# Kernel optimization log

Measured on AMD Instinct MI355X. Metric: run time of the kernel, lower is better.

## Reference

```python
import jax, jax.numpy as jnp
import numpy as np


def _hardswish(x):
    return x * jnp.clip(x + 3.0, 0.0, 6.0) / 6.0


def _rel_coords_table(W):
    # [1, 2W-1, 2W-1, 2], log-spaced continuous relative coords (SwinV2)
    rc = jnp.arange(-(W - 1), W, dtype=jnp.float32)
    grid = jnp.stack(jnp.meshgrid(rc, rc, indexing='ij'), axis=-1)[None]
    grid = grid / float(W - 1) * 8.0
    return jnp.sign(grid) * jnp.log2(jnp.abs(grid) + 1.0) / np.float32(np.log2(8.0))


def _rel_pos_index(W):
    # [N, N] int indices into the (2W-1)^2 bias table
    coords = np.stack(np.meshgrid(np.arange(W), np.arange(W), indexing='ij')).reshape(2, -1)
    rel = (coords[:, :, None] - coords[:, None, :]).transpose(1, 2, 0)  # [N, N, 2]
    rel[:, :, 0] += W - 1
    rel[:, :, 1] += W - 1
    rel[:, :, 0] *= 2 * W - 1
    return jnp.asarray(rel.sum(-1))


def setup_inputs() -> dict:
    key = jax.random.key(0)
    ks = jax.random.split(key, 6)
    dim, num_heads, W = 512, 16, 8
    N = W * W
    B, nW = 2048, 64
    return {
        'x': jax.random.normal(ks[0], (B, N, dim), jnp.float32),
        'mask': jax.random.normal(ks[1], (nW, N, N), jnp.float32),
        'w_qkv': jax.random.normal(ks[2], (dim, 3 * dim), jnp.float32) * 0.02,
        'w_out': jax.random.normal(ks[3], (dim, dim), jnp.float32) * 0.02,
        'cpb_w1': jax.random.normal(ks[4], (2, 512), jnp.float32) * 0.02,
        'cpb_w2': jax.random.normal(ks[5], (512, num_heads), jnp.float32) * 0.02,
        'logits_scale': jnp.log(10.0 * jnp.ones((num_heads, 1, 1), jnp.float32)),
        'window_size': W,
        'num_heads': num_heads,
    }


def reference(x, mask, w_qkv, w_out, cpb_w1, cpb_w2, logits_scale, window_size, num_heads):
    B, N, C = x.shape
    hd = C // num_heads
    qkv = (x @ w_qkv).reshape(B, N, 3, num_heads, hd).transpose(2, 0, 3, 1, 4)
    q, k, v = qkv[0], qkv[1], qkv[2]  # [B, H, N, hd]

    # cosine attention (L2-normalized q, k) with clamped learned logit scale
    qn = q / jnp.clip(jnp.linalg.norm(q, axis=-1, keepdims=True), 1e-12)
    kn = k / jnp.clip(jnp.linalg.norm(k, axis=-1, keepdims=True), 1e-12)
    attn = jnp.einsum('bhnd,bhmd->bhnm', qn, kn)
    scale = jnp.exp(jnp.minimum(logits_scale, jnp.log(jnp.float32(100.0))))  # [H,1,1]
    attn = attn * scale[None]

    # continuous position bias via tiny MLP + index gather, sigmoid-scaled
    table = _rel_coords_table(window_size)                       # [1, 2W-1, 2W-1, 2]
    bias_table = (_hardswish(table @ cpb_w1) @ cpb_w2).reshape(-1, num_heads)
    idx = _rel_pos_index(window_size)                            # [N, N]
    bias = bias_table[idx.reshape(-1)].reshape(N, N, num_heads).transpose(2, 0, 1)
    attn = attn + 16.0 * jax.nn.sigmoid(bias)[None]

    if mask is not None:
        nW = mask.shape[0]
        attn = attn.reshape(B // nW, nW, num_heads, N, N) + mask[None, :, None]
        attn = attn.reshape(B, num_heads, N, N)

    # NOTE: original uses nn.Softmax(1) -> softmax over the HEAD axis; replicate faithfully
    attn = jax.nn.softmax(attn, axis=1)

    out = jnp.einsum('bhnm,bhmd->bhnd', attn, v).transpose(0, 2, 1, 3).reshape(B, N, C)
    return out @ w_out
```

## Files before the change

### kernel.cpp

```cpp
#include <hip/hip_runtime.h>
#include <hip/hip_bf16.h>

typedef unsigned short u16;
typedef unsigned int u32;
typedef __attribute__((ext_vector_type(8))) short bf16x8;
typedef __attribute__((ext_vector_type(4))) float f32x4;
typedef __attribute__((ext_vector_type(4))) float float4v;

__device__ __forceinline__ float bf2f(u16 v) {
  union { u32 u; float f; } x; x.u = ((u32)v) << 16; return x.f;
}
__device__ __forceinline__ u16 f2bf(float f) {
  union { u32 u; float f; } x; x.f = f;
  return (u16)((x.u + 0x7fffu + ((x.u >> 16) & 1u)) >> 16);
}

__device__ __forceinline__ void gload16(const void* g, void* l) {
  __builtin_amdgcn_global_load_lds(
      (const __attribute__((address_space(1))) u32*)g,
      (__attribute__((address_space(3))) u32*)l, 16, 0, 0);
}

#define MFMA16(a, bfr, cacc) __builtin_amdgcn_mfma_f32_16x16x32_bf16((a), (bfr), (cacc), 0, 0, 0)


__global__ void transpose_kernel(const float* __restrict__ in, u16* __restrict__ out,
                                 int R, int C) {
  int t = blockIdx.x * blockDim.x + threadIdx.x;
  if (t >= R * C) return;
  int c = t / R, r = t % R;
  out[t] = f2bf(in[r * C + c]);
}

__global__ void wqkv_swz_kernel(const float* __restrict__ w, u16* __restrict__ out) {
  int t = blockIdx.x * blockDim.x + threadIdx.x;
  if (t >= 48 * 16384) return;
  int whead = t >> 14;
  int rest = t & 16383;
  int chunk = rest >> 7;
  int kk = chunk >> 3, dt = (chunk >> 2) & 1, lg = chunk & 3;
  int li = (rest >> 3) & 15, e = rest & 7;
  int s = whead >> 4, h = whead & 15;
  out[t] = f2bf(w[(size_t)(kk * 32 + lg * 8 + e) * 1536 + s * 512 + h * 32 + dt * 16 + li]);
}

__global__ void bias_tab_kernel(const float* __restrict__ w1, const float* __restrict__ w2,
                                float* __restrict__ tab) {
  int t = blockIdx.x * blockDim.x + threadIdx.x;
  if (t >= 225 * 16) return;
  int r = t >> 4, h = t & 15;
  int i = r / 15, j = r % 15;
  float gi = (float)(i - 7) * (8.0f / 7.0f);
  float gj = (float)(j - 7) * (8.0f / 7.0f);
  float si = (gi > 0.f) ? 1.f : ((gi < 0.f) ? -1.f : 0.f);
  float sj = (gj > 0.f) ? 1.f : ((gj < 0.f) ? -1.f : 0.f);
  float t0 = si * log2f(fabsf(gi) + 1.0f) * (1.0f / 3.0f);
  float t1 = sj * log2f(fabsf(gj) + 1.0f) * (1.0f / 3.0f);
  float acc = 0.f;
  for (int k = 0; k < 512; ++k) {
    float a = t0 * w1[k] + t1 * w1[512 + k];
    float hs = a * fminf(fmaxf(a + 3.f, 0.f), 6.f) * (1.f / 6.f);
    acc += hs * w2[k * 16 + h];
  }
  tab[t] = acc;
}

__global__ void bias16_kernel(const float* __restrict__ tab, float* __restrict__ b16) {
  int t = blockIdx.x * blockDim.x + threadIdx.x;
  if (t >= 16 * 64 * 64) return;
  int h = t >> 12, nm = t & 4095, n = nm >> 6, m = nm & 63;
  int idx = ((n >> 3) - (m >> 3) + 7) * 15 + ((n & 7) - (m & 7) + 7);
  float b = tab[idx * 16 + h];
  b16[t] = 16.0f / (1.0f + expf(-b));
}

template <bool F32OUT>
__global__ __launch_bounds__(256) void gemm_bt(const u16* __restrict__ A,
                                               const u16* __restrict__ Bt,
                                               void* __restrict__ Cout,
                                               int M, int N, int K) {
  __shared__ u16 lA[128 * 64];
  __shared__ u16 lB[128 * 64];
  const int tid = threadIdx.x;
  const int w = tid >> 6, l = tid & 63;
  const int lg = l >> 4, li = l & 15;
  const int nbn = N >> 7;
  const int nwg = gridDim.x;
  int bidx = blockIdx.x;
  int q = nwg >> 3, r = nwg & 7;
  int xcd = bidx & 7, pos = bidx >> 3;
  int swz = (xcd < r ? xcd * (q + 1) : r * (q + 1) + (xcd - r) * q) + pos;
  int bm = swz / nbn, bn = swz % nbn;
  const int wr = w >> 1, wc = w & 1;

  f32x4 acc[4][4];
#pragma unroll
  for (int i = 0; i < 4; i++)
#pragma unroll
    for (int j = 0; j < 4; j++) acc[i][j] = (f32x4){0.f, 0.f, 0.f, 0.f};

  const u16* Abase = A + (size_t)(bm * 128) * K;
  const u16* Bbase = Bt + (size_t)(bn * 128) * K;

  for (int k0 = 0; k0 < K; k0 += 64) {
#pragma unroll
    for (int i = 0; i < 4; ++i) {
      int c = w * 256 + i * 64 + l;
      int row = c >> 3, kc = c & 7;
      gload16(Abase + (size_t)row * K + k0 + kc * 8, (u16*)lA + c * 8);
      gload16(Bbase + (size_t)row * K + k0 + kc * 8, (u16*)lB + c * 8);
    }
    __syncthreads();
#pragma unroll
    for (int kk = 0; kk < 2; ++kk) {
      bf16x8 af[4], bfr[4];
#pragma unroll
      for (int t = 0; t < 4; ++t) {
        int row = wr * 64 + t * 16 + li;
        af[t] = *(const bf16x8*)&lA[row * 64 + kk * 32 + lg * 8];
        int col = wc * 64 + t * 16 + li;
        bfr[t] = *(const bf16x8*)&lB[col * 64 + kk * 32 + lg * 8];
      }
#pragma unroll
      for (int tm = 0; tm < 4; ++tm)
#pragma unroll
        for (int tn = 0; tn < 4; ++tn)
          acc[tm][tn] = MFMA16(af[tm], bfr[tn], acc[tm][tn]);
    }
    __syncthreads();
  }
  int r0 = bm * 128 + wr * 64 + lg * 4;
  int c0 = bn * 128 + wc * 64 + li;
#pragma unroll
  for (int tm = 0; tm < 4; ++tm)
#pragma unroll
    for (int tn = 0; tn < 4; ++tn)
#pragma unroll
      for (int j = 0; j < 4; ++j) {
        size_t off = (size_t)(r0 + tm * 16 + j) * N + c0 + tn * 16;
        if (F32OUT)
          ((float*)Cout)[off] = acc[tm][tn][j];
        else
          ((u16*)Cout)[off] = f2bf(acc[tm][tn][j]);
      }
}

__global__ __launch_bounds__(1024)
__attribute__((amdgpu_waves_per_eu(4, 4))) void fused_attn(
    const float* __restrict__ x, const float* __restrict__ mask,
    const u16* __restrict__ wqkv2, const float* __restrict__ bias16,
    const float* __restrict__ lscale, u16* __restrict__ aout) {
  __shared__ float S[33280];
  u16* xl = (u16*)S;
  u16* bb = xl + 32768;
  float* ob = S;
  u16* P16 = (u16*)S;

  const int tid = threadIdx.x;
  const int h = tid >> 6, l = tid & 63;
  const int lg = l >> 4, li = l & 15;
  const int b = blockIdx.x, wm = b & 63;
  const float* xg = x + (size_t)b * 64 * 512;

  {
    int n = tid >> 4, seg = tid & 15;
    const float4v* src = (const float4v*)(xg + n * 512 + seg * 32);
#pragma unroll
    for (int i = 0; i < 4; ++i) {
      float4v a = src[2 * i], c = src[2 * i + 1];
      union { bf16x8 v; u16 s[8]; } o;
      o.s[0] = f2bf(a[0]); o.s[1] = f2bf(a[1]); o.s[2] = f2bf(a[2]); o.s[3] = f2bf(a[3]);
      o.s[4] = f2bf(c[0]); o.s[5] = f2bf(c[1]); o.s[6] = f2bf(c[2]); o.s[7] = f2bf(c[3]);
      *(bf16x8*)(xl + ((n * 64 + ((seg * 4 + i) ^ (n & 7))) << 3)) = o.v;
    }
  }
  float sc = __expf(fminf(lscale[h], 4.6051702f));
  __syncthreads();

  bf16x8 qf[4], kf[4];

  {
    f32x4 qa[4][2], ka[4][2];
#pragma unroll
    for (int rt = 0; rt < 4; ++rt)
#pragma unroll
      for (int dt = 0; dt < 2; ++dt) {
        qa[rt][dt] = (f32x4){0.f, 0.f, 0.f, 0.f};
        ka[rt][dt] = (f32x4){0.f, 0.f, 0.f, 0.f};
      }
    const u16* bq2 = wqkv2 + (size_t)h * 16384;
    const u16* bk2 = wqkv2 + (size_t)(16 + h) * 16384;
#pragma unroll
    for (int kk = 0; kk < 16; ++kk) {
      bf16x8 ax[4];
#pragma unroll
      for (int rt = 0; rt < 4; ++rt) {
        int n = rt * 16 + li;
        ax[rt] = *(const bf16x8*)(xl + ((n * 64 + ((kk * 4 + lg) ^ (n & 7))) << 3));
      }
#pragma unroll
      for (int dt = 0; dt < 2; ++dt) {
        int coff = (kk * 2 + dt) * 512 + lg * 128 + li * 8;
        bf16x8 fq = *(const bf16x8*)(bq2 + coff);
        bf16x8 fk = *(const bf16x8*)(bk2 + coff);
#pragma unroll
        for (int rt = 0; rt < 4; ++rt) {
          qa[rt][dt] = MFMA16(ax[rt], fq, qa[rt][dt]);
          ka[rt][dt] = MFMA16(ax[rt], fk, ka[rt][dt]);
        }
      }
    }
#pragma unroll
    for (int rt = 0; rt < 4; ++rt) {
      f32x4 q2, k2;
#pragma unroll
      for (int j = 0; j < 4; ++j) {
        q2[j] = qa[rt][0][j] * qa[rt][0][j] + qa[rt][1][j] * qa[rt][1][j];
        k2[j] = ka[rt][0][j] * ka[rt][0][j] + ka[rt][1][j] * ka[rt][1][j];
      }
#pragma unroll
      for (int s = 1; s <= 8; s <<= 1)
#pragma unroll
        for (int j = 0; j < 4; ++j) {
          q2[j] += __shfl_xor(q2[j], s);
          k2[j] += __shfl_xor(k2[j], s);
        }
#pragma unroll
      for (int j = 0; j < 4; ++j) {
        float rq = sc / fmaxf(sqrtf(q2[j]), 1e-12f);
        float rk = 1.0f / fmaxf(sqrtf(k2[j]), 1e-12f);
#pragma unroll
        for (int dt = 0; dt < 2; ++dt) {
          qa[rt][dt][j] *= rq;
          ka[rt][dt][j] *= rk;
        }
      }
    }
#pragma unroll
    for (int rt = 0; rt < 4; ++rt)
#pragma unroll
      for (int dt = 0; dt < 2; ++dt)
#pragma unroll
        for (int j = 0; j < 4; ++j) {
          int n = rt * 16 + lg * 4 + j;
          int d = dt * 16 + li;
          int s = (n ^ (n >> 2)) & 3;
          bb[h * 2048 + n * 32 + (((d >> 3) ^ s) << 3) + (d & 7)] = f2bf(qa[rt][dt][j]);
        }
    __syncthreads();
#pragma unroll
    for (int t = 0; t < 4; ++t) {
      int n = t * 16 + li;
      int s = (n ^ (n >> 2)) & 3;
      qf[t] = *(const bf16x8*)(bb + h * 2048 + n * 32 + ((lg ^ s) << 3));
    }
    __syncthreads();
#pragma unroll
    for (int rt = 0; rt < 4; ++rt)
#pragma unroll
      for (int dt = 0; dt < 2; ++dt)
#pragma unroll
        for (int j = 0; j < 4; ++j) {
          int n = rt * 16 + lg * 4 + j;
          int d = dt * 16 + li;
          int s = (n ^ (n >> 2)) & 3;
          bb[h * 2048 + n * 32 + (((d >> 3) ^ s) << 3) + (d & 7)] = f2bf(ka[rt][dt][j]);
        }
    __syncthreads();
#pragma unroll
    for (int t = 0; t < 4; ++t) {
      int n = t * 16 + li;
      int s = (n ^ (n >> 2)) & 3;
      kf[t] = *(const bf16x8*)(bb + h * 2048 + n * 32 + ((lg ^ s) << 3));
    }
  }

  f32x4 va[4][2];
#pragma unroll
  for (int rt = 0; rt < 4; ++rt)
#pragma unroll
    for (int dt = 0; dt < 2; ++dt) va[rt][dt] = (f32x4){0.f, 0.f, 0.f, 0.f};
  {
    const u16* bv2 = wqkv2 + (size_t)(32 + h) * 16384;
#pragma unroll
    for (int kk = 0; kk < 16; ++kk) {
      bf16x8 ax[4];
#pragma unroll
      for (int rt = 0; rt < 4; ++rt) {
        int n = rt * 16 + li;
        ax[rt] = *(const bf16x8*)(xl + ((n * 64 + ((kk * 4 + lg) ^ (n & 7))) << 3));
      }
#pragma unroll
      for (int dt = 0; dt < 2; ++dt) {
        bf16x8 fv = *(const bf16x8*)(bv2 + (kk * 2 + dt) * 512 + lg * 128 + li * 8);
#pragma unroll
        for (int rt = 0; rt < 4; ++rt) va[rt][dt] = MFMA16(ax[rt], fv, va[rt][dt]);
      }
    }
  }
  __syncthreads();

  const float* bias_h = bias16 + h * 4096;
  const float* mask_w = mask + wm * 4096;
  f32x4 oacc[4][2];
#pragma unroll
  for (int i = 0; i < 4; i++) {
    oacc[i][0] = (f32x4){0.f, 0.f, 0.f, 0.f};
    oacc[i][1] = (f32x4){0.f, 0.f, 0.f, 0.f};
  }

#pragma unroll
  for (int c = 0; c < 2; ++c) {
#pragma unroll
    for (int tn = 0; tn < 4; ++tn)
#pragma unroll
      for (int t = 0; t < 2; ++t) {
        int mt = c * 2 + t;
        f32x4 z = {0.f, 0.f, 0.f, 0.f};
        f32x4 s = MFMA16(qf[tn], kf[mt], z);
        int mloc = t * 16 + li;
        int mg = c * 32 + mloc;
#pragma unroll
        for (int j = 0; j < 4; ++j) {
          int n = tn * 16 + lg * 4 + j;
          S[h * 2080 + mloc * 65 + n] = s[j] + bias_h[n * 64 + mg] + mask_w[n * 64 + mg];
        }
      }
    __syncthreads();
#pragma unroll
    for (int pp = 0; pp < 2; ++pp) {
      int p = tid + pp * 1024;
      int base = (p >> 6) * 65 + (p & 63);
      float mx = -3.0e38f;
#pragma unroll
      for (int hh = 0; hh < 16; ++hh) mx = fmaxf(mx, S[hh * 2080 + base]);
      float sum = 0.f;
#pragma unroll
      for (int hh = 0; hh < 16; ++hh) {
        float e = __expf(S[hh * 2080 + base] - mx);
        S[hh * 2080 + base] = e;
        sum += e;
      }
      float inv = 1.0f / sum;
#pragma unroll
      for (int hh = 0; hh < 16; ++hh)
        P16[(hh * 2080 + base) * 2] = f2bf(S[hh * 2080 + base] * inv);
    }
    __syncthreads();
    bf16x8 vf[2];
#pragma unroll
    for (int td = 0; td < 2; ++td)
#pragma unroll
      for (int j = 0; j < 8; ++j) {
        int srcl = (((lg * 2 + (j >> 2)) & 3) << 4) + li;
        float a0 = __shfl(va[c * 2][td][j & 3], srcl);
        float a1 = __shfl(va[c * 2 + 1][td][j & 3], srcl);
        vf[td][j] = (short)f2bf(lg >= 2 ? a1 : a0);
      }
#pragma unroll
    for (int tn = 0; tn < 4; ++tn) {
      bf16x8 pf;
#pragma unroll
      for (int e = 0; e < 8; ++e)
        pf[e] = (short)P16[(h * 2080 + (lg * 8 + e) * 65 + tn * 16 + li) * 2];
      oacc[tn][0] = MFMA16(pf, vf[0], oacc[tn][0]);
      oacc[tn][1] = MFMA16(pf, vf[1], oacc[tn][1]);
    }
    __syncthreads();
  }

#pragma unroll
  for (int tn = 0; tn < 4; ++tn)
#pragma unroll
    for (int td = 0; td < 2; ++td)
#pragma unroll
      for (int j = 0; j < 4; ++j) {
        int n = tn * 16 + lg * 4 + j;
        ob[n * 516 + h * 32 + td * 16 + li] = oacc[tn][td][j];
      }
  __syncthreads();
  {
    int n = tid >> 4, seg = tid & 15;
    u16* dst = aout + ((size_t)b * 64 + n) * 512 + seg * 32;
    const float* srcr = ob + n * 516 + seg * 32;
#pragma unroll
    for (int i = 0; i < 4; ++i) {
      union { bf16x8 v; u16 s[8]; } o;
#pragma unroll
      for (int e = 0; e < 8; ++e) o.s[e] = f2bf(srcr[i * 8 + e]);
      *(bf16x8*)(dst + i * 8) = o.v;
    }
  }
}

extern "C" void kernel_launch(void* const* d_in, const int* in_sizes, int n_in,
                              void* d_out, int out_size, void* d_ws, size_t ws_size,
                              hipStream_t stream) {
  const float* x = (const float*)d_in[0];
  const float* mask = (const float*)d_in[1];
  const float* w_qkv = (const float*)d_in[2];
  const float* w_out = (const float*)d_in[3];
  const float* cpb_w1 = (const float*)d_in[4];
  const float* cpb_w2 = (const float*)d_in[5];
  const float* lscale = (const float*)d_in[6];
  float* out = (float*)d_out;

  char* ws = (char*)d_ws;
  u16* wqkv2 = (u16*)ws;
  u16* woutT = (u16*)(ws + 1572864ull);
  float* btab = (float*)(ws + 2097152ull);
  float* b16 = (float*)(ws + 2113536ull);
  u16* attn_out = (u16*)(ws + 2375680ull);

  wqkv_swz_kernel<<<(48 * 16384) / 256, 256, 0, stream>>>(w_qkv, wqkv2);
  transpose_kernel<<<(512 * 512 + 255) / 256, 256, 0, stream>>>(w_out, woutT, 512, 512);
  bias_tab_kernel<<<(225 * 16 + 255) / 256, 256, 0, stream>>>(cpb_w1, cpb_w2, btab);
  bias16_kernel<<<(16 * 64 * 64 + 255) / 256, 256, 0, stream>>>(btab, b16);

  fused_attn<<<2048, 1024, 0, stream>>>(x, mask, wqkv2, b16, lscale, attn_out);

  gemm_bt<true><<<4096, 256, 0, stream>>>(attn_out, woutT, out, 131072, 512, 512);
}
```

Before: 942.6 us.

## Process two heads per wave in fused attention with 512-thread blocks

Halves the fused attention block from 1024 to 512 threads, with each wave now computing two heads (w and w+8). The QKV projection reuses each LDS x fragment across both heads' MFMAs. The launch bound becomes (512, 2) so two blocks can share a CU, letting one block's barriers overlap with another's work. The cost is doubled per-wave register state (q/k/v/o accumulators for two heads), which risks spills or lower occupancy, and LDS usage per block (~133KB) may itself prevent two blocks from co-residing.

```diff
diff --git a/kernel.cpp b/kernel.cpp
--- a/kernel.cpp
+++ b/kernel.cpp
@@ -145,8 +145,7 @@
       }
 }
 
-__global__ __launch_bounds__(1024)
-__attribute__((amdgpu_waves_per_eu(4, 4))) void fused_attn(
+__global__ __launch_bounds__(512, 2) void fused_attn(
     const float* __restrict__ x, const float* __restrict__ mask,
     const u16* __restrict__ wqkv2, const float* __restrict__ bias16,
     const float* __restrict__ lscale, u16* __restrict__ aout) {
@@ -157,39 +156,42 @@
   u16* P16 = (u16*)S;
 
   const int tid = threadIdx.x;
-  const int h = tid >> 6, l = tid & 63;
+  const int w = tid >> 6, l = tid & 63;
   const int lg = l >> 4, li = l & 15;
   const int b = blockIdx.x, wm = b & 63;
   const float* xg = x + (size_t)b * 64 * 512;
 
   {
-    int n = tid >> 4, seg = tid & 15;
-    const float4v* src = (const float4v*)(xg + n * 512 + seg * 32);
-#pragma unroll
-    for (int i = 0; i < 4; ++i) {
+    int n = tid >> 3, seg = tid & 7;
+    const float4v* src = (const float4v*)(xg + n * 512 + seg * 64);
+#pragma unroll
+    for (int i = 0; i < 8; ++i) {
       float4v a = src[2 * i], c = src[2 * i + 1];
       union { bf16x8 v; u16 s[8]; } o;
       o.s[0] = f2bf(a[0]); o.s[1] = f2bf(a[1]); o.s[2] = f2bf(a[2]); o.s[3] = f2bf(a[3]);
       o.s[4] = f2bf(c[0]); o.s[5] = f2bf(c[1]); o.s[6] = f2bf(c[2]); o.s[7] = f2bf(c[3]);
-      *(bf16x8*)(xl + ((n * 64 + ((seg * 4 + i) ^ (n & 7))) << 3)) = o.v;
-    }
-  }
-  float sc = __expf(fminf(lscale[h], 4.6051702f));
+      *(bf16x8*)(xl + ((n * 64 + ((seg * 8 + i) ^ (n & 7))) << 3)) = o.v;
+    }
+  }
+  float sc[2];
+#pragma unroll
+  for (int hp = 0; hp < 2; ++hp)
+    sc[hp] = __expf(fminf(lscale[w + hp * 8], 4.6051702f));
   __syncthreads();
 
-  bf16x8 qf[4], kf[4];
+  bf16x8 qf[2][4], kf[2][4];
 
   {
-    f32x4 qa[4][2], ka[4][2];
-#pragma unroll
-    for (int rt = 0; rt < 4; ++rt)
-#pragma unroll
-      for (int dt = 0; dt < 2; ++dt) {
-        qa[rt][dt] = (f32x4){0.f, 0.f, 0.f, 0.f};
-        ka[rt][dt] = (f32x4){0.f, 0.f, 0.f, 0.f};
-      }
-    const u16* bq2 = wqkv2 + (size_t)h * 16384;
-    const u16* bk2 = wqkv2 + (size_t)(16 + h) * 16384;
+    f32x4 qa[2][4][2], ka[2][4][2];
+#pragma unroll
+    for (int hp = 0; hp < 2; ++hp)
+#pragma unroll
+      for (int rt = 0; rt < 4; ++rt)
+#pragma unroll
+        for (int dt = 0; dt < 2; ++dt) {
+          qa[hp][rt][dt] = (f32x4){0.f, 0.f, 0.f, 0.f};
+          ka[hp][rt][dt] = (f32x4){0.f, 0.f, 0.f, 0.f};
+        }
 #pragma unroll
     for (int kk = 0; kk < 16; ++kk) {
       bf16x8 ax[4];
@@ -201,87 +203,110 @@
 #pragma unroll
       for (int dt = 0; dt < 2; ++dt) {
         int coff = (kk * 2 + dt) * 512 + lg * 128 + li * 8;
-        bf16x8 fq = *(const bf16x8*)(bq2 + coff);
-        bf16x8 fk = *(const bf16x8*)(bk2 + coff);
-#pragma unroll
-        for (int rt = 0; rt < 4; ++rt) {
-          qa[rt][dt] = MFMA16(ax[rt], fq, qa[rt][dt]);
-          ka[rt][dt] = MFMA16(ax[rt], fk, ka[rt][dt]);
-        }
-      }
-    }
-#pragma unroll
-    for (int rt = 0; rt < 4; ++rt) {
-      f32x4 q2, k2;
-#pragma unroll
-      for (int j = 0; j < 4; ++j) {
-        q2[j] = qa[rt][0][j] * qa[rt][0][j] + qa[rt][1][j] * qa[rt][1][j];
-        k2[j] = ka[rt][0][j] * ka[rt][0][j] + ka[rt][1][j] * ka[rt][1][j];
-      }
-#pragma unroll
-      for (int s = 1; s <= 8; s <<= 1)
+#pragma unroll
+        for (int hp = 0; hp < 2; ++hp) {
+          int h = w + hp * 8;
+          bf16x8 fq = *(const bf16x8*)(wqkv2 + (size_t)h * 16384 + coff);
+          bf16x8 fk = *(const bf16x8*)(wqkv2 + (size_t)(16 + h) * 16384 + coff);
+#pragma unroll
+          for (int rt = 0; rt < 4; ++rt) {
+            qa[hp][rt][dt] = MFMA16(ax[rt], fq, qa[hp][rt][dt]);
+            ka[hp][rt][dt] = MFMA16(ax[rt], fk, ka[hp][rt][dt]);
+          }
+        }
+      }
+    }
+#pragma unroll
+    for (int hp = 0; hp < 2; ++hp)
+#pragma unroll
+      for (int rt = 0; rt < 4; ++rt) {
+        f32x4 q2, k2;
 #pragma unroll
         for (int j = 0; j < 4; ++j) {
-          q2[j] += __shfl_xor(q2[j], s);
-          k2[j] += __shfl_xor(k2[j], s);
-        }
-#pragma unroll
-      for (int j = 0; j < 4; ++j) {
-        float rq = sc / fmaxf(sqrtf(q2[j]), 1e-12f);
-        float rk = 1.0f / fmaxf(sqrtf(k2[j]), 1e-12f);
-#pragma unroll
-        for (int dt = 0; dt < 2; ++dt) {
-          qa[rt][dt][j] *= rq;
-          ka[rt][dt][j] *= rk;
-        }
-      }
-    }
+          q2[j] = qa[hp][rt][0][j] * qa[hp][rt][0][j] + qa[hp][rt][1][j] * qa[hp][rt][1][j];
+          k2[j] = ka[hp][rt][0][j] * ka[hp][rt][0][j] + ka[hp][rt][1][j] * ka[hp][rt][1][j];
+        }
+#pragma unroll
+        for (int s = 1; s <= 8; s <<= 1)
+#pragma unroll
+          for (int j = 0; j < 4; ++j) {
+            q2[j] += __shfl_xor(q2[j], s);
+            k2[j] += __shfl_xor(k2[j], s);
+          }
+#pragma unroll
+        for (int j = 0; j < 4; ++j) {
+          float rq = sc[hp] / fmaxf(sqrtf(q2[j]), 1e-12f);
+          float rk = 1.0f / fmaxf(sqrtf(k2[j]), 1e-12f);
+#pragma unroll
+          for (int dt = 0; dt < 2; ++dt) {
+            qa[hp][rt][dt][j] *= rq;
+            ka[hp][rt][dt][j] *= rk;
+          }
+        }
+      }
+#pragma unroll
+    for (int hp = 0; hp < 2; ++hp) {
+      int h = w + hp * 8;
+#pragma unroll
+      for (int rt = 0; rt < 4; ++rt)
+#pragma unroll
+        for (int dt = 0; dt < 2; ++dt)
+#pragma unroll
+          for (int j = 0; j < 4; ++j) {
+            int n = rt * 16 + lg * 4 + j;
+            int d = dt * 16 + li;
+            int s = (n ^ (n >> 2)) & 3;
+            bb[h * 2048 + n * 32 + (((d >> 3) ^ s) << 3) + (d & 7)] = f2bf(qa[hp][rt][dt][j]);
+          }
+    }
+    __syncthreads();
+#pragma unroll
+    for (int hp = 0; hp < 2; ++hp) {
+      int h = w + hp * 8;
+#pragma unroll
+      for (int t = 0; t < 4; ++t) {
+        int n = t * 16 + li;
+        int s = (n ^ (n >> 2)) & 3;
+        qf[hp][t] = *(const bf16x8*)(bb + h * 2048 + n * 32 + ((lg ^ s) << 3));
+      }
+    }
+    __syncthreads();
+#pragma unroll
+    for (int hp = 0; hp < 2; ++hp) {
+      int h = w + hp * 8;
+#pragma unroll
+      for (int rt = 0; rt < 4; ++rt)
+#pragma unroll
+        for (int dt = 0; dt < 2; ++dt)
+#pragma unroll
+          for (int j = 0; j < 4; ++j) {
+            int n = rt * 16 + lg * 4 + j;
+            int d = dt * 16 + li;
+            int s = (n ^ (n >> 2)) & 3;
+            bb[h * 2048 + n * 32 + (((d >> 3) ^ s) << 3) + (d & 7)] = f2bf(ka[hp][rt][dt][j]);
+          }
+    }
+    __syncthreads();
+#pragma unroll
+    for (int hp = 0; hp < 2; ++hp) {
+      int h = w + hp * 8;
+#pragma unroll
+      for (int t = 0; t < 4; ++t) {
+        int n = t * 16 + li;
+        int s = (n ^ (n >> 2)) & 3;
+        kf[hp][t] = *(const bf16x8*)(bb + h * 2048 + n * 32 + ((lg ^ s) << 3));
+      }
+    }
+  }
+
+  f32x4 va[2][4][2];
+#pragma unroll
+  for (int hp = 0; hp < 2; ++hp)
 #pragma unroll
     for (int rt = 0; rt < 4; ++rt)
 #pragma unroll
-      for (int dt = 0; dt < 2; ++dt)
-#pragma unroll
-        for (int j = 0; j < 4; ++j) {
-          int n = rt * 16 + lg * 4 + j;
-          int d = dt * 16 + li;
-          int s = (n ^ (n >> 2)) & 3;
-          bb[h * 2048 + n * 32 + (((d >> 3) ^ s) << 3) + (d & 7)] = f2bf(qa[rt][dt][j]);
-        }
-    __syncthreads();
-#pragma unroll
-    for (int t = 0; t < 4; ++t) {
-      int n = t * 16 + li;
-      int s = (n ^ (n >> 2)) & 3;
-      qf[t] = *(const bf16x8*)(bb + h * 2048 + n * 32 + ((lg ^ s) << 3));
-    }
-    __syncthreads();
-#pragma unroll
-    for (int rt = 0; rt < 4; ++rt)
-#pragma unroll
-      for (int dt = 0; dt < 2; ++dt)
-#pragma unroll
-        for (int j = 0; j < 4; ++j) {
-          int n = rt * 16 + lg * 4 + j;
-          int d = dt * 16 + li;
-          int s = (n ^ (n >> 2)) & 3;
-          bb[h * 2048 + n * 32 + (((d >> 3) ^ s) << 3) + (d & 7)] = f2bf(ka[rt][dt][j]);
-        }
-    __syncthreads();
-#pragma unroll
-    for (int t = 0; t < 4; ++t) {
-      int n = t * 16 + li;
-      int s = (n ^ (n >> 2)) & 3;
-      kf[t] = *(const bf16x8*)(bb + h * 2048 + n * 32 + ((lg ^ s) << 3));
-    }
-  }
-
-  f32x4 va[4][2];
-#pragma unroll
-  for (int rt = 0; rt < 4; ++rt)
-#pragma unroll
-    for (int dt = 0; dt < 2; ++dt) va[rt][dt] = (f32x4){0.f, 0.f, 0.f, 0.f};
+      for (int dt = 0; dt < 2; ++dt) va[hp][rt][dt] = (f32x4){0.f, 0.f, 0.f, 0.f};
   {
-    const u16* bv2 = wqkv2 + (size_t)(32 + h) * 16384;
 #pragma unroll
     for (int kk = 0; kk < 16; ++kk) {
       bf16x8 ax[4];
@@ -292,44 +317,55 @@
       }
 #pragma unroll
       for (int dt = 0; dt < 2; ++dt) {
-        bf16x8 fv = *(const bf16x8*)(bv2 + (kk * 2 + dt) * 512 + lg * 128 + li * 8);
-#pragma unroll
-        for (int rt = 0; rt < 4; ++rt) va[rt][dt] = MFMA16(ax[rt], fv, va[rt][dt]);
+        int coff = (kk * 2 + dt) * 512 + lg * 128 + li * 8;
+#pragma unroll
+        for (int hp = 0; hp < 2; ++hp) {
+          int h = w + hp * 8;
+          bf16x8 fv = *(const bf16x8*)(wqkv2 + (size_t)(32 + h) * 16384 + coff);
+#pragma unroll
+          for (int rt = 0; rt < 4; ++rt) va[hp][rt][dt] = MFMA16(ax[rt], fv, va[hp][rt][dt]);
+        }
       }
     }
   }
   __syncthreads();
 
-  const float* bias_h = bias16 + h * 4096;
   const float* mask_w = mask + wm * 4096;
-  f32x4 oacc[4][2];
-#pragma unroll
-  for (int i = 0; i < 4; i++) {
-    oacc[i][0] = (f32x4){0.f, 0.f, 0.f, 0.f};
-    oacc[i][1] = (f32x4){0.f, 0.f, 0.f, 0.f};
-  }
+  f32x4 oacc[2][4][2];
+#pragma unroll
+  for (int hp = 0; hp < 2; ++hp)
+#pragma unroll
+    for (int i = 0; i < 4; i++) {
+      oacc[hp][i][0] = (f32x4){0.f, 0.f, 0.f, 0.f};
+      oacc[hp][i][1] = (f32x4){0.f, 0.f, 0.f, 0.f};
+    }
 
 #pragma unroll
   for (int c = 0; c < 2; ++c) {
 #pragma unroll
-    for (int tn = 0; tn < 4; ++tn)
-#pragma unroll
-      for (int t = 0; t < 2; ++t) {
-        int mt = c * 2 + t;
-        f32x4 z = {0.f, 0.f, 0.f, 0.f};
-        f32x4 s = MFMA16(qf[tn], kf[mt], z);
-        int mloc = t * 16 + li;
-        int mg = c * 32 + mloc;
-#pragma unroll
-        for (int j = 0; j < 4; ++j) {
-          int n = tn * 16 + lg * 4 + j;
-          S[h * 2080 + mloc * 65 + n] = s[j] + bias_h[n * 64 + mg] + mask_w[n * 64 + mg];
-        }
-      }
-    __syncthreads();
-#pragma unroll
-    for (int pp = 0; pp < 2; ++pp) {
-      int p = tid + pp * 1024;
+    for (int hp = 0; hp < 2; ++hp) {
+      int h = w + hp * 8;
+      const float* bias_h = bias16 + h * 4096;
+#pragma unroll
+      for (int tn = 0; tn < 4; ++tn)
+#pragma unroll
+        for (int t = 0; t < 2; ++t) {
+          int mt = c * 2 + t;
+          f32x4 z = {0.f, 0.f, 0.f, 0.f};
+          f32x4 s = MFMA16(qf[hp][tn], kf[hp][mt], z);
+          int mloc = t * 16 + li;
+          int mg = c * 32 + mloc;
+#pragma unroll
+          for (int j = 0; j < 4; ++j) {
+            int n = tn * 16 + lg * 4 + j;
+            S[h * 2080 + mloc * 65 + n] = s[j] + bias_h[n * 64 + mg] + mask_w[n * 64 + mg];
+          }
+        }
+    }
+    __syncthreads();
+#pragma unroll
+    for (int pp = 0; pp < 4; ++pp) {
+      int p = tid + pp * 512;
       int base = (p >> 6) * 65 + (p & 63);
       float mx = -3.0e38f;
 #pragma unroll
@@ -347,44 +383,52 @@
         P16[(hh * 2080 + base) * 2] = f2bf(S[hh * 2080 + base] * inv);
     }
     __syncthreads();
-    bf16x8 vf[2];
-#pragma unroll
-    for (int td = 0; td < 2; ++td)
-#pragma unroll
-      for (int j = 0; j < 8; ++j) {
-        int srcl = (((lg * 2 + (j >> 2)) & 3) << 4) + li;
-        float a0 = __shfl(va[c * 2][td][j & 3], srcl);
-        float a1 = __shfl(va[c * 2 + 1][td][j & 3], srcl);
-        vf[td][j] = (short)f2bf(lg >= 2 ? a1 : a0);
-      }
-#pragma unroll
-    for (int tn = 0; tn < 4; ++tn) {
-      bf16x8 pf;
-#pragma unroll
-      for (int e = 0; e < 8; ++e)
-        pf[e] = (short)P16[(h * 2080 + (lg * 8 + e) * 65 + tn * 16 + li) * 2];
-      oacc[tn][0] = MFMA16(pf, vf[0], oacc[tn][0]);
-      oacc[tn][1] = MFMA16(pf, vf[1], oacc[tn][1]);
-    }
-    __syncthreads();
-  }
-
-#pragma unroll
-  for (int tn = 0; tn < 4; ++tn)
-#pragma unroll
-    for (int td = 0; td < 2; ++td)
-#pragma unroll
-      for (int j = 0; j < 4; ++j) {
-        int n = tn * 16 + lg * 4 + j;
-        ob[n * 516 + h * 32 + td * 16 + li] = oacc[tn][td][j];
-      }
+#pragma unroll
+    for (int hp = 0; hp < 2; ++hp) {
+      int h = w + hp * 8;
+      bf16x8 vf[2];
+#pragma unroll
+      for (int td = 0; td < 2; ++td)
+#pragma unroll
+        for (int j = 0; j < 8; ++j) {
+          int srcl = (((lg * 2 + (j >> 2)) & 3) << 4) + li;
+          float a0 = __shfl(va[hp][c * 2][td][j & 3], srcl);
+          float a1 = __shfl(va[hp][c * 2 + 1][td][j & 3], srcl);
+          vf[td][j] = (short)f2bf(lg >= 2 ? a1 : a0);
+        }
+#pragma unroll
+      for (int tn = 0; tn < 4; ++tn) {
+        bf16x8 pf;
+#pragma unroll
+        for (int e = 0; e < 8; ++e)
+          pf[e] = (short)P16[(h * 2080 + (lg * 8 + e) * 65 + tn * 16 + li) * 2];
+        oacc[hp][tn][0] = MFMA16(pf, vf[0], oacc[hp][tn][0]);
+        oacc[hp][tn][1] = MFMA16(pf, vf[1], oacc[hp][tn][1]);
+      }
+    }
+    __syncthreads();
+  }
+
+#pragma unroll
+  for (int hp = 0; hp < 2; ++hp) {
+    int h = w + hp * 8;
+#pragma unroll
+    for (int tn = 0; tn < 4; ++tn)
+#pragma unroll
+      for (int td = 0; td < 2; ++td)
+#pragma unroll
+        for (int j = 0; j < 4; ++j) {
+          int n = tn * 16 + lg * 4 + j;
+          ob[n * 516 + h * 32 + td * 16 + li] = oacc[hp][tn][td][j];
+        }
+  }
   __syncthreads();
   {
-    int n = tid >> 4, seg = tid & 15;
-    u16* dst = aout + ((size_t)b * 64 + n) * 512 + seg * 32;
-    const float* srcr = ob + n * 516 + seg * 32;
-#pragma unroll
-    for (int i = 0; i < 4; ++i) {
+    int n = tid >> 3, seg = tid & 7;
+    u16* dst = aout + ((size_t)b * 64 + n) * 512 + seg * 64;
+    const float* srcr = ob + n * 516 + seg * 64;
+#pragma unroll
+    for (int i = 0; i < 8; ++i) {
       union { bf16x8 v; u16 s[8]; } o;
 #pragma unroll
       for (int e = 0; e < 8; ++e) o.s[e] = f2bf(srcr[i * 8 + e]);
@@ -417,7 +461,7 @@
   bias_tab_kernel<<<(225 * 16 + 255) / 256, 256, 0, stream>>>(cpb_w1, cpb_w2, btab);
   bias16_kernel<<<(16 * 64 * 64 + 255) / 256, 256, 0, stream>>>(btab, b16);
 
-  fused_attn<<<2048, 1024, 0, stream>>>(x, mask, wqkv2, b16, lscale, attn_out);
+  fused_attn<<<2048, 512, 0, stream>>>(x, mask, wqkv2, b16, lscale, attn_out);
 
   gemm_bt<true><<<4096, 256, 0, stream>>>(attn_out, woutT, out, 131072, 512, 512);
 }
```

After: 1.036 ms. 9.9% more time.
